# Performance work log

Measured on AMD Instinct MI355X. Metric: run time of the kernel, lower is better.

## Reference

```python
import jax, jax.numpy as jnp
import numpy as np

N, E, F_IN, H, C, G, NC = 10000, 160000, 512, 8, 64, 64, 64


def setup_inputs() -> dict:
    key = jax.random.key(0)
    ks = jax.random.split(key, 16)
    d = {}
    d['x'] = jax.random.normal(ks[0], (N, F_IN), jnp.float32)
    d['edge_index'] = jax.random.randint(ks[1], (2, E), 0, N, dtype=jnp.int32)
    d['batch'] = jnp.sort(jax.random.randint(ks[2], (N,), 0, G, dtype=jnp.int32))
    s = 0.05
    d['enc_W'] = jax.random.normal(ks[3], (F_IN, H * C), jnp.float32) * s
    d['enc_b'] = jnp.zeros((H * C,), jnp.float32)
    d['W1'] = jax.random.normal(ks[4], (H * C, H * C), jnp.float32) * s
    d['as1'] = jax.random.normal(ks[5], (H, C), jnp.float32) * s
    d['ad1'] = jax.random.normal(ks[6], (H, C), jnp.float32) * s
    d['b1'] = jnp.zeros((H * C,), jnp.float32)
    d['g1'] = jnp.ones((H * C,), jnp.float32)
    d['be1'] = jnp.zeros((H * C,), jnp.float32)
    d['W2'] = jax.random.normal(ks[7], (H * C, H * C), jnp.float32) * s
    d['as2'] = jax.random.normal(ks[8], (H, C), jnp.float32) * s
    d['ad2'] = jax.random.normal(ks[9], (H, C), jnp.float32) * s
    d['b2'] = jnp.zeros((H * C,), jnp.float32)
    d['g2'] = jnp.ones((H * C,), jnp.float32)
    d['be2'] = jnp.zeros((H * C,), jnp.float32)
    d['W3'] = jax.random.normal(ks[10], (H * C, C), jnp.float32) * s
    d['as3'] = jax.random.normal(ks[11], (1, C), jnp.float32) * s
    d['ad3'] = jax.random.normal(ks[12], (1, C), jnp.float32) * s
    d['b3'] = jnp.zeros((C,), jnp.float32)
    d['g3'] = jnp.ones((C,), jnp.float32)
    d['be3'] = jnp.zeros((C,), jnp.float32)
    d['lin_W'] = jax.random.normal(ks[13], (C, NC), jnp.float32) * s
    d['lin_b'] = jnp.zeros((NC,), jnp.float32)
    return d


def _gat_conv(x, src, dst, W, a_s, a_d, bias, concat):
    # PyG GATConv (eval mode, self-loops already appended to src/dst)
    n = x.shape[0]
    heads, c = a_s.shape
    h = (x @ W).reshape(n, heads, c)                      # [N,H,C]
    logits = (h * a_s).sum(-1)[src] + (h * a_d).sum(-1)[dst]  # [E',H]
    logits = jax.nn.leaky_relu(logits, 0.2)
    m = jax.ops.segment_max(logits, dst, num_segments=n)  # segment softmax over dst
    e = jnp.exp(logits - m[dst])
    s = jax.ops.segment_sum(e, dst, num_segments=n)
    alpha = e / (s[dst] + 1e-16)                          # [E',H]
    out = jax.ops.segment_sum(alpha[:, :, None] * h[src], dst, num_segments=n)
    out = out.reshape(n, heads * c) if concat else out.mean(axis=1)
    return out + bias


def _bn(x, g, b):
    # BatchNorm1d, training-mode statistics (biased var), eps=1e-5
    mu = x.mean(axis=0)
    var = ((x - mu) ** 2).mean(axis=0)
    return g * (x - mu) / jnp.sqrt(var + 1e-5) + b


def reference(x, edge_index, batch, enc_W, enc_b,
              W1, as1, ad1, b1, g1, be1,
              W2, as2, ad2, b2, g2, be2,
              W3, as3, ad3, b3, g3, be3,
              lin_W, lin_b):
    n = x.shape[0]
    loops = jnp.arange(n, dtype=edge_index.dtype)
    src = jnp.concatenate([edge_index[0], loops])
    dst = jnp.concatenate([edge_index[1], loops])
    x = x @ enc_W + enc_b
    # layer 1 (concat heads) + bn + elu + residual
    h = x
    x = _gat_conv(x, src, dst, W1, as1, ad1, b1, True)
    x = jax.nn.elu(_bn(x, g1, be1))
    x = h + x
    # layer 2
    h = x
    x = _gat_conv(x, src, dst, W2, as2, ad2, b2, True)
    x = jax.nn.elu(_bn(x, g2, be2))
    x = h + x
    # layer 3 (heads=1, mean/no-concat), bn, no elu, no residual (shape mismatch)
    x = _gat_conv(x, src, dst, W3, as3, ad3, b3, False)
    x = _bn(x, g3, be3)
    # global mean pool over graphs
    sums = jax.ops.segment_sum(x, batch, num_segments=G)
    cnt = jax.ops.segment_sum(jnp.ones((n,), x.dtype), batch, num_segments=G)
    xg = sums / jnp.clip(cnt, 1.0)[:, None]
    return xg @ lin_W + lin_b
```

## Files before the change

kernel.cpp:

```cpp
#include <hip/hip_runtime.h>
#include <hip/hip_bf16.h>
#include <math.h>

#define NNODES 10000
#define RPAD   10240
#define MPAD   10112
#define EDGES  160000
#define EPLUS  170000
#define FIN    512
#define HEADS8 8
#define CH     64
#define HC     512
#define NG     64
#define NCLS   64
#define NSTAT  256
#define NSTAT3 64

typedef _Float16 f16x8 __attribute__((ext_vector_type(8)));
typedef _Float16 f16x4 __attribute__((ext_vector_type(4)));
typedef _Float16 f16x2 __attribute__((ext_vector_type(2)));
typedef float    f32x4 __attribute__((ext_vector_type(4)));

#define GLD_LDS16(g, l)                                                        \
    __builtin_amdgcn_global_load_lds(                                          \
        (const __attribute__((address_space(1))) void*)(g),                    \
        (__attribute__((address_space(3))) void*)(l), 16, 0, 0)

#define PREP_CNT  665
#define PREP_CONV 5000
__global__ void prep_all(const int* __restrict__ ei, int* __restrict__ deg,
                         const int* __restrict__ batch, int* __restrict__ goff,
                         const float* __restrict__ x_in, _Float16* __restrict__ x16,
                         const float* __restrict__ Wa, const float* __restrict__ Wb,
                         const float* __restrict__ Wc, const float* __restrict__ Wd,
                         _Float16* __restrict__ Ta, _Float16* __restrict__ Tb,
                         _Float16* __restrict__ Tc, _Float16* __restrict__ Td,
                         _Float16* __restrict__ g16pad, float* __restrict__ g3opad)
{
    const int b   = blockIdx.x;
    const int tid = threadIdx.x;
    if (b < PREP_CNT) {
        const float4 z4 = make_float4(0.f, 0.f, 0.f, 0.f);
        if (b < 60)
            ((float4*)g16pad)[b * 256 + tid] = z4;
        else if (b < 75)
            ((float4*)g3opad)[(b - 60) * 256 + tid] = z4;
        int e = b * 256 + tid;
        if (e < NNODES) {
            int bb = batch[e];
            int bprev = (e == 0) ? -1 : batch[e - 1];
            for (int g = bprev + 1; g <= bb; ++g) goff[g] = e;
            if (e == NNODES - 1)
                for (int g = bb + 1; g <= NG; ++g) goff[g] = NNODES;
        }
        if (e >= EPLUS) return;
        int dst = (e < EDGES) ? ei[EDGES + e] : (e - EDGES);
        atomicAdd(&deg[dst], 1);
    } else if (b < PREP_CNT + PREP_CONV) {
        int i = (b - PREP_CNT) * 256 + tid;
        float4 v = ((const float4*)x_in)[i];
        f16x4 o;
        o[0] = (_Float16)v.x; o[1] = (_Float16)v.y;
        o[2] = (_Float16)v.z; o[3] = (_Float16)v.w;
        ((f16x4*)x16)[i] = o;
    } else {
        int tb = b - (PREP_CNT + PREP_CONV);
        int z  = tb >> 8;
        int rem = tb & 255;
        int bxi = rem & 15, byi = rem >> 4;
        if (z == 3 && bxi >= 2) return;
        const float* W = (z == 0) ? Wa : (z == 1) ? Wb : (z == 2) ? Wc : Wd;
        _Float16*    T = (z == 0) ? Ta : (z == 1) ? Tb : (z == 2) ? Tc : Td;
        const int ldW = (z == 3) ? 64 : 512;
        __shared__ float t[32][33];
        int bx = bxi * 32, by = byi * 32;
        int tx = tid & 31, ty = tid >> 5;
        #pragma unroll
        for (int i = 0; i < 32; i += 8)
            t[ty + i][tx] = W[(size_t)(by + ty + i) * ldW + bx + tx];
        __syncthreads();
        #pragma unroll
        for (int i = 0; i < 32; i += 8)
            T[(size_t)(bx + ty + i) * 512 + by + tx] = (_Float16)t[tx][ty + i];
    }
}

__device__ void exscan_dev(const int* __restrict__ deg, int* __restrict__ off,
                           int* __restrict__ cursor, int* partial )
{
    const int tid = threadIdx.x;
    const int chunk = (NNODES + 255) / 256;
    int begin = tid * chunk;
    int end   = begin + chunk; if (end > NNODES) end = NNODES;
    if (begin > NNODES) begin = NNODES;
    int s = 0;
    for (int i = begin; i < end; ++i) s += deg[i];
    partial[tid] = s;
    __syncthreads();
    for (int o = 1; o < 256; o <<= 1) {
        int v = (tid >= o) ? partial[tid - o] : 0;
        __syncthreads();
        partial[tid] += v;
        __syncthreads();
    }
    int run = (tid > 0) ? partial[tid - 1] : 0;
    for (int i = begin; i < end; ++i) {
        off[i] = run; cursor[i] = run; run += deg[i];
    }
    if (tid == 255) off[NNODES] = run;
}

__global__ __launch_bounds__(256) void gemm_f16_mfma(
    const _Float16* __restrict__ A16, const _Float16* __restrict__ Bt16,
    const float* __restrict__ bias, _Float16* __restrict__ C16,
    float* __restrict__ ssrc, float* __restrict__ sdst,
    const float* __restrict__ a_s, const float* __restrict__ a_d,
    int Mt, int Nn, int K,
    int tail, const int* __restrict__ tp0, int* __restrict__ tp1,
    int* __restrict__ tp2)
{
    __shared__ _Float16 As[128 * 32] __attribute__((aligned(16)));
    __shared__ _Float16 Bs[64 * 32]  __attribute__((aligned(16)));
    __shared__ float sS[2][128];
    __shared__ float sD[2][128];
    const int tid  = threadIdx.x;
    const int ncols = Nn >> 6;
    const int nb    = ncols * (Mt >> 7);
    const int bid   = blockIdx.x;

    if (bid >= nb) {
        if (tail == 1) {
            exscan_dev(tp0, tp1, tp2, (int*)As);
        } else if (tail == 2) {
            int e = (bid - nb) * 256 + tid;
            if (e < EPLUS) {
                int srcN, dstN;
                if (e < EDGES) { srcN = tp0[e]; dstN = tp0[EDGES + e]; }
                else           { srcN = dstN = e - EDGES; }
                int pos = atomicAdd(&tp1[dstN], 1);
                tp2[pos] = srcN;
            }
        }
        return;
    }

    const int bt   = bid % ncols;
    const int row0 = (bid / ncols) * 128;
    const int col0 = bt * 64;
    const int wave = tid >> 6;
    const int lane = tid & 63;
    const int wy = wave >> 1, wx = wave & 1;

    const int lrow = lane >> 2;
    const int lk   = (lane & 3) * 8;

    f32x4 acc[4][2] = {};

    for (int k0 = 0; k0 < K; k0 += 32) {
        if (k0) __syncthreads();
        #pragma unroll
        for (int r = 0; r < 2; ++r) {
            const int chunk = r * 4 + wave;
            const int trow  = chunk * 16 + lrow;
            GLD_LDS16(A16 + (size_t)(row0 + trow) * K + k0 + lk,
                      &As[chunk * 512]);
        }
        {
            const int trow = wave * 16 + lrow;
            GLD_LDS16(Bt16 + (size_t)(col0 + trow) * K + k0 + lk,
                      &Bs[wave * 512]);
        }
        __syncthreads();

        const int quad = lane >> 4;
        const int l16  = lane & 15;
        f16x8 af[4], bf[2];
        #pragma unroll
        for (int m = 0; m < 4; ++m)
            af[m] = *(const f16x8*)&As[(wy * 64 + m * 16 + l16) * 32 + quad * 8];
        #pragma unroll
        for (int n = 0; n < 2; ++n)
            bf[n] = *(const f16x8*)&Bs[(wx * 32 + n * 16 + l16) * 32 + quad * 8];
        #pragma unroll
        for (int m = 0; m < 4; ++m)
            #pragma unroll
            for (int n = 0; n < 2; ++n)
                acc[m][n] = __builtin_amdgcn_mfma_f32_16x16x32_f16(
                    af[m], bf[n], acc[m][n], 0, 0, 0);
    }

    const int quad = lane >> 4;
    const int l16  = lane & 15;
    #pragma unroll
    for (int m = 0; m < 4; ++m) {
        #pragma unroll
        for (int n = 0; n < 2; ++n) {
            const int col = col0 + wx * 32 + n * 16 + l16;
            const float bv = bias ? bias[col] : 0.0f;
            #pragma unroll
            for (int r = 0; r < 4; ++r) {
                const int row = row0 + wy * 64 + m * 16 + quad * 4 + r;
                C16[(size_t)row * Nn + col] = (_Float16)(acc[m][n][r] + bv);
            }
        }
    }

    if (ssrc) {
        float a_sv[2], a_dv[2];
        #pragma unroll
        for (int n = 0; n < 2; ++n) {
            const int col = col0 + wx * 32 + n * 16 + l16;
            a_sv[n] = a_s[col & 511];
            a_dv[n] = a_d[col & 511];
        }
        #pragma unroll
        for (int m = 0; m < 4; ++m) {
            #pragma unroll
            for (int r = 0; r < 4; ++r) {
                float vs = acc[m][0][r] * a_sv[0] + acc[m][1][r] * a_sv[1];
                float vd = acc[m][0][r] * a_dv[0] + acc[m][1][r] * a_dv[1];
                vs += __shfl_xor(vs, 1); vs += __shfl_xor(vs, 2);
                vs += __shfl_xor(vs, 4); vs += __shfl_xor(vs, 8);
                vd += __shfl_xor(vd, 1); vd += __shfl_xor(vd, 2);
                vd += __shfl_xor(vd, 4); vd += __shfl_xor(vd, 8);
                if (l16 == 0) {
                    const int lr = wy * 64 + m * 16 + quad * 4 + r;
                    sS[wx][lr] = vs;
                    sD[wx][lr] = vd;
                }
            }
        }
        __syncthreads();
        if (wx == 0 && l16 == 0) {
            const int head = bt;
            #pragma unroll
            for (int m = 0; m < 4; ++m)
                #pragma unroll
                for (int r = 0; r < 4; ++r) {
                    const int lr = wy * 64 + m * 16 + quad * 4 + r;
                    const int row = row0 + lr;
                    ssrc[(size_t)row * HEADS8 + head] = sS[0][lr] + sS[1][lr];
                    sdst[(size_t)row * HEADS8 + head] = sD[0][lr] + sD[1][lr];
                }
        }
    }
}

__global__ __launch_bounds__(256) void gemm_f16_mfma_n64(
    const _Float16* __restrict__ A16, const _Float16* __restrict__ Bt16,
    _Float16* __restrict__ C16,
    float* __restrict__ ssrc, float* __restrict__ sdst,
    const float* __restrict__ a_s, const float* __restrict__ a_d)
{
    __shared__ _Float16 As[64 * 32] __attribute__((aligned(16)));
    __shared__ _Float16 Bs[64 * 32] __attribute__((aligned(16)));
    __shared__ float sS[2][64];
    __shared__ float sD[2][64];
    const int tid  = threadIdx.x;
    const int wave = tid >> 6;
    const int lane = tid & 63;
    const int row0 = blockIdx.x * 64;
    const int wy = wave >> 1, wx = wave & 1;

    const int lrow = lane >> 2;
    const int lk   = (lane & 3) * 8;

    f32x4 acc[2][2] = {};

    for (int k0 = 0; k0 < 512; k0 += 32) {
        if (k0) __syncthreads();
        {
            const int trow = wave * 16 + lrow;
            GLD_LDS16(A16 + (size_t)(row0 + trow) * 512 + k0 + lk, &As[wave * 512]);
            GLD_LDS16(Bt16 + (size_t)trow * 512 + k0 + lk, &Bs[wave * 512]);
        }
        __syncthreads();

        const int quad = lane >> 4;
        const int l16  = lane & 15;
        f16x8 af[2], bf[2];
        #pragma unroll
        for (int m = 0; m < 2; ++m)
            af[m] = *(const f16x8*)&As[(wy * 32 + m * 16 + l16) * 32 + quad * 8];
        #pragma unroll
        for (int n = 0; n < 2; ++n)
            bf[n] = *(const f16x8*)&Bs[(wx * 32 + n * 16 + l16) * 32 + quad * 8];
        #pragma unroll
        for (int m = 0; m < 2; ++m)
            #pragma unroll
            for (int n = 0; n < 2; ++n)
                acc[m][n] = __builtin_amdgcn_mfma_f32_16x16x32_f16(
                    af[m], bf[n], acc[m][n], 0, 0, 0);
    }

    const int quad = lane >> 4;
    const int l16  = lane & 15;
    #pragma unroll
    for (int m = 0; m < 2; ++m)
        #pragma unroll
        for (int n = 0; n < 2; ++n) {
            const int col = wx * 32 + n * 16 + l16;
            #pragma unroll
            for (int r = 0; r < 4; ++r) {
                const int row = row0 + wy * 32 + m * 16 + quad * 4 + r;
                C16[(size_t)row * 64 + col] = (_Float16)acc[m][n][r];
            }
        }

    {
        float a_sv[2], a_dv[2];
        #pragma unroll
        for (int n = 0; n < 2; ++n) {
            const int col = wx * 32 + n * 16 + l16;
            a_sv[n] = a_s[col];
            a_dv[n] = a_d[col];
        }
        #pragma unroll
        for (int m = 0; m < 2; ++m)
            #pragma unroll
            for (int r = 0; r < 4; ++r) {
                float vs = acc[m][0][r] * a_sv[0] + acc[m][1][r] * a_sv[1];
                float vd = acc[m][0][r] * a_dv[0] + acc[m][1][r] * a_dv[1];
                vs += __shfl_xor(vs, 1); vs += __shfl_xor(vs, 2);
                vs += __shfl_xor(vs, 4); vs += __shfl_xor(vs, 8);
                vd += __shfl_xor(vd, 1); vd += __shfl_xor(vd, 2);
                vd += __shfl_xor(vd, 4); vd += __shfl_xor(vd, 8);
                if (l16 == 0) {
                    const int lr = wy * 32 + m * 16 + quad * 4 + r;
                    sS[wx][lr] = vs;
                    sD[wx][lr] = vd;
                }
            }
        __syncthreads();
        if (wx == 0 && l16 == 0) {
            #pragma unroll
            for (int m = 0; m < 2; ++m)
                #pragma unroll
                for (int r = 0; r < 4; ++r) {
                    const int lr = wy * 32 + m * 16 + quad * 4 + r;
                    const int row = row0 + lr;
                    ssrc[row] = sS[0][lr] + sS[1][lr];
                    sdst[row] = sD[0][lr] + sD[1][lr];
                }
        }
    }
}

__global__ __launch_bounds__(64) void gat_aggregate8(
    const _Float16* __restrict__ Hf, const float* __restrict__ ssrc,
    const float* __restrict__ sdst, const int* __restrict__ off,
    const int* __restrict__ csr, const float* __restrict__ bias,
    _Float16* __restrict__ out)
{
    const int n    = blockIdx.x;
    const int lane = threadIdx.x;
    const int head = lane >> 3;
    const int e0 = off[n], e1 = off[n + 1];

    float4 sd0 = ((const float4*)(sdst + n * 8))[0];
    float4 sd1 = ((const float4*)(sdst + n * 8))[1];
    float sd[8] = {sd0.x, sd0.y, sd0.z, sd0.w, sd1.x, sd1.y, sd1.z, sd1.w};

    __shared__ float exL[64 * 8];
    __shared__ int   srcL[64];
    float acc[8]  = {};
    float ssum[8] = {};
    for (int base = e0; base < e1; base += 64) {
        int cnt = e1 - base; if (cnt > 64) cnt = 64;
        if (lane < cnt) {
            int s = csr[base + lane];
            srcL[lane] = s;
            float4 s0 = ((const float4*)(ssrc + s * 8))[0];
            float4 s1 = ((const float4*)(ssrc + s * 8))[1];
            float lv[8] = {s0.x, s0.y, s0.z, s0.w, s1.x, s1.y, s1.z, s1.w};
            #pragma unroll
            for (int h = 0; h < 8; ++h) {
                float l = lv[h] + sd[h];
                l = (l > 0.f) ? l : 0.2f * l;
                float ex = __expf(l);
                exL[lane * 8 + h] = ex;
                ssum[h] += ex;
            }
        }
        __syncthreads();
        int j = 0;
        for (; j + 4 <= cnt; j += 4) {
            const int s0 = srcL[j],     s1 = srcL[j + 1];
            const int s2 = srcL[j + 2], s3 = srcL[j + 3];
            f16x8 h0 = *(const f16x8*)(Hf + (size_t)s0 * HC + lane * 8);
            f16x8 h1 = *(const f16x8*)(Hf + (size_t)s1 * HC + lane * 8);
            f16x8 h2 = *(const f16x8*)(Hf + (size_t)s2 * HC + lane * 8);
            f16x8 h3 = *(const f16x8*)(Hf + (size_t)s3 * HC + lane * 8);
            const float a0 = exL[(j)     * 8 + head];
            const float a1 = exL[(j + 1) * 8 + head];
            const float a2 = exL[(j + 2) * 8 + head];
            const float a3 = exL[(j + 3) * 8 + head];
            #pragma unroll
            for (int c = 0; c < 8; ++c) {
                acc[c] = fmaf(a0, (float)h0[c], acc[c]);
                acc[c] = fmaf(a1, (float)h1[c], acc[c]);
                acc[c] = fmaf(a2, (float)h2[c], acc[c]);
                acc[c] = fmaf(a3, (float)h3[c], acc[c]);
            }
        }
        for (; j < cnt; ++j) {
            const int s = srcL[j];
            f16x8 hv = *(const f16x8*)(Hf + (size_t)s * HC + lane * 8);
            const float al = exL[j * 8 + head];
            #pragma unroll
            for (int c = 0; c < 8; ++c)
                acc[c] = fmaf(al, (float)hv[c], acc[c]);
        }
        __syncthreads();
    }
    #pragma unroll
    for (int h = 0; h < 8; ++h)
        #pragma unroll
        for (int o = 1; o < 64; o <<= 1)
            ssum[h] += __shfl_xor(ssum[h], o);

    const float inv = 1.0f / (ssum[head] + 1e-16f);
    const float* bp = bias + lane * 8;
    f16x8 ov;
    #pragma unroll
    for (int c = 0; c < 8; ++c)
        ov[c] = (_Float16)(acc[c] * inv + bp[c]);
    *(f16x8*)(out + (size_t)n * HC + lane * 8) = ov;
}

__global__ __launch_bounds__(64) void gat_aggregate1(
    const _Float16* __restrict__ Hf, const float* __restrict__ ssrc,
    const float* __restrict__ sdst, const int* __restrict__ off,
    const int* __restrict__ csr, const float* __restrict__ bias,
    float* __restrict__ out)
{
    const int n    = blockIdx.x;
    const int lane = threadIdx.x;
    const int e0 = off[n], e1 = off[n + 1];
    const float sd = sdst[n];

    __shared__ float exL[64];
    __shared__ int   srcL[64];
    float acc = 0.f, ssum = 0.f;
    for (int base = e0; base < e1; base += 64) {
        int cnt = e1 - base; if (cnt > 64) cnt = 64;
        if (lane < cnt) {
            int s = csr[base + lane];
            srcL[lane] = s;
            float l = ssrc[s] + sd;
            l = (l > 0.f) ? l : 0.2f * l;
            float ex = __expf(l);
            exL[lane] = ex;
            ssum += ex;
        }
        __syncthreads();
        int j = 0;
        for (; j + 4 <= cnt; j += 4) {
            const int s0 = srcL[j],     s1 = srcL[j + 1];
            const int s2 = srcL[j + 2], s3 = srcL[j + 3];
            float h0 = (float)Hf[(size_t)s0 * 64 + lane];
            float h1 = (float)Hf[(size_t)s1 * 64 + lane];
            float h2 = (float)Hf[(size_t)s2 * 64 + lane];
            float h3 = (float)Hf[(size_t)s3 * 64 + lane];
            acc = fmaf(exL[j],     h0, acc);
            acc = fmaf(exL[j + 1], h1, acc);
            acc = fmaf(exL[j + 2], h2, acc);
            acc = fmaf(exL[j + 3], h3, acc);
        }
        for (; j < cnt; ++j)
            acc = fmaf(exL[j], (float)Hf[(size_t)srcL[j] * 64 + lane], acc);
        __syncthreads();
    }
    #pragma unroll
    for (int o = 1; o < 64; o <<= 1)
        ssum += __shfl_xor(ssum, o);

    out[(size_t)n * 64 + lane] = acc / (ssum + 1e-16f) + bias[lane];
}

__global__ __launch_bounds__(256) void bn_stats_f16(
    const _Float16* __restrict__ x,
    float* __restrict__ psum, float* __restrict__ psq)
{
    const int t    = threadIdx.x;
    const int lane = t & 63;
    const int wv   = t >> 6;
    const int w    = blockIdx.x * 4 + wv;
    float s[8] = {}, q[8] = {};
    #pragma unroll
    for (int k = 0; k < RPAD / 2048; ++k) {
        const int r0 = w + k * 2048;
        f16x8 v0 = *(const f16x8*)(x + (size_t)r0 * HC + lane * 8);
        f16x8 v1 = *(const f16x8*)(x + (size_t)(r0 + 1024) * HC + lane * 8);
        #pragma unroll
        for (int j = 0; j < 8; ++j) {
            float f0 = (float)v0[j], f1 = (float)v1[j];
            s[j] += f0 + f1;
            q[j] += f0 * f0 + f1 * f1;
        }
    }
    __shared__ float ls[4][HC];
    __shared__ float lq[4][HC];
    #pragma unroll
    for (int j = 0; j < 8; ++j) {
        ls[wv][lane * 8 + j] = s[j];
        lq[wv][lane * 8 + j] = q[j];
    }
    __syncthreads();
    const size_t bo = (size_t)blockIdx.x * HC;
    #pragma unroll
    for (int k = 0; k < 2; ++k) {
        const int ch = t + k * 256;
        psum[bo + ch] = ls[0][ch] + ls[1][ch] + ls[2][ch] + ls[3][ch];
        psq [bo + ch] = lq[0][ch] + lq[1][ch] + lq[2][ch] + lq[3][ch];
    }
}

__global__ __launch_bounds__(256) void bn_stats3(
    const float* __restrict__ x,
    float* __restrict__ psum, float* __restrict__ psq)
{
    const int t    = threadIdx.x;
    const int c4   = (t & 15) * 4;
    const int rsub = t >> 4;
    float s[4] = {}, q[4] = {};
    #pragma unroll
    for (int k = 0; k < RPAD / 1024; ++k) {
        const int r = blockIdx.x * 16 + rsub + k * 1024;
        float4 v = *(const float4*)(x + (size_t)r * CH + c4);
        s[0] += v.x; q[0] += v.x * v.x;
        s[1] += v.y; q[1] += v.y * v.y;
        s[2] += v.z; q[2] += v.z * v.z;
        s[3] += v.w; q[3] += v.w * v.w;
    }
    __shared__ float ls[16][CH];
    __shared__ float lq[16][CH];
    #pragma unroll
    for (int j = 0; j < 4; ++j) {
        ls[rsub][c4 + j] = s[j];
        lq[rsub][c4 + j] = q[j];
    }
    __syncthreads();
    if (t < CH) {
        float tot = 0.f;
        #pragma unroll
        for (int p = 0; p < 16; ++p) tot += ls[p][t];
        psum[(size_t)blockIdx.x * CH + t] = tot;
    } else if (t < 2 * CH) {
        const int ch = t - CH;
        float tot = 0.f;
        #pragma unroll
        for (int p = 0; p < 16; ++p) tot += lq[p][ch];
        psq[(size_t)blockIdx.x * CH + ch] = tot;
    }
}

__global__ __launch_bounds__(256) void bn_finalize(
    const float* __restrict__ psum, const float* __restrict__ psq,
    const float* __restrict__ g, const float* __restrict__ be,
    float* __restrict__ scale, float* __restrict__ shift,
    float invN, int cols, int np)
{
    const int t  = threadIdx.x;
    const int pg = t >> 4;
    const int cl = t & 15;
    const int ch = blockIdx.x * 16 + cl;
    float S = 0.f, Q = 0.f;
    for (int p = pg; p < np; p += 16) {
        S += psum[(size_t)p * cols + ch];
        Q += psq [(size_t)p * cols + ch];
    }
    __shared__ float lsS[16][16];
    __shared__ float lsQ[16][16];
    lsS[pg][cl] = S;
    lsQ[pg][cl] = Q;
    __syncthreads();
    if (t < 16) {
        float S2 = 0.f, Q2 = 0.f;
        #pragma unroll
        for (int p = 0; p < 16; ++p) { S2 += lsS[p][t]; Q2 += lsQ[p][t]; }
        const int c = blockIdx.x * 16 + t;
        float mu  = S2 * invN;
        float var = Q2 * invN - mu * mu;
        float sc  = g[c] / sqrtf(var + 1e-5f);
        scale[c] = sc;
        shift[c] = be[c] - mu * sc;
    }
}

__global__ void bn_apply16(const _Float16* __restrict__ xin,
                           const _Float16* __restrict__ res,
                           const float* __restrict__ scale,
                           const float* __restrict__ shift,
                           _Float16* __restrict__ out, size_t total8)
{
    size_t i = (size_t)blockIdx.x * blockDim.x + threadIdx.x;
    if (i >= total8) return;
    int c = (int)((i * 8) & (size_t)(HC - 1));
    f16x8 xv = ((const f16x8*)xin)[i];
    f16x8 rv = ((const f16x8*)res)[i];
    float4 sa = *(const float4*)(scale + c);
    float4 sb = *(const float4*)(scale + c + 4);
    float4 ha = *(const float4*)(shift + c);
    float4 hb = *(const float4*)(shift + c + 4);
    float sc[8] = {sa.x, sa.y, sa.z, sa.w, sb.x, sb.y, sb.z, sb.w};
    float sh[8] = {ha.x, ha.y, ha.z, ha.w, hb.x, hb.y, hb.z, hb.w};
    f16x8 o;
    #pragma unroll
    for (int j = 0; j < 8; ++j) {
        float v = (float)xv[j] * sc[j] + sh[j];
        v = (v > 0.f) ? v : expm1f(v);
        o[j] = (_Float16)(v + (float)rv[j]);
    }
    ((f16x8*)out)[i] = o;
}

__global__ __launch_bounds__(256) void pool_linear(
    const float* __restrict__ x, const int* __restrict__ goff,
    const float* __restrict__ W, const float* __restrict__ b,
    const float* __restrict__ scale, const float* __restrict__ shift,
    float* __restrict__ out)
{
    const int g    = blockIdx.x;
    const int lane = threadIdx.x & 63;
    const int wave = threadIdx.x >> 6;
    const int r0 = goff[g], r1 = goff[g + 1];
    float s = 0.f;
    for (int r = r0 + wave; r < r1; r += 4)
        s += x[(size_t)r * CH + lane];
    __shared__ float red[4][CH];
    __shared__ float mean_l[CH];
    red[wave][lane] = s;
    __syncthreads();
    if (wave == 0) {
        float tot = red[0][lane] + red[1][lane] + red[2][lane] + red[3][lane];
        float cnt = (float)(r1 - r0);
        float m = tot / fmaxf(cnt, 1.0f);
        mean_l[lane] = m * scale[lane] + shift[lane];
    }
    __syncthreads();
    if (threadIdx.x < NCLS) {
        const int j = threadIdx.x;
        float acc = b[j];
        for (int c = 0; c < CH; ++c)
            acc = fmaf(mean_l[c], W[c * NCLS + j], acc);
        out[g * NCLS + j] = acc;
    }
}

extern "C" void kernel_launch(void* const* d_in, const int* in_sizes, int n_in,
                              void* d_out, int out_size, void* d_ws, size_t ws_size,
                              hipStream_t stream)
{
    const float* x_in  = (const float*)d_in[0];
    const int*   ei    = (const int*)  d_in[1];
    const int*   batch = (const int*)  d_in[2];
    const float* enc_W = (const float*)d_in[3];
    const float* enc_b = (const float*)d_in[4];
    const float* W1  = (const float*)d_in[5];
    const float* as1 = (const float*)d_in[6];
    const float* ad1 = (const float*)d_in[7];
    const float* b1  = (const float*)d_in[8];
    const float* g1  = (const float*)d_in[9];
    const float* be1 = (const float*)d_in[10];
    const float* W2  = (const float*)d_in[11];
    const float* as2 = (const float*)d_in[12];
    const float* ad2 = (const float*)d_in[13];
    const float* b2  = (const float*)d_in[14];
    const float* g2  = (const float*)d_in[15];
    const float* be2 = (const float*)d_in[16];
    const float* W3  = (const float*)d_in[17];
    const float* as3 = (const float*)d_in[18];
    const float* ad3 = (const float*)d_in[19];
    const float* b3  = (const float*)d_in[20];
    const float* g3  = (const float*)d_in[21];
    const float* be3 = (const float*)d_in[22];
    const float* linW = (const float*)d_in[23];
    const float* linb = (const float*)d_in[24];
    float* out = (float*)d_out;

    char* ws = (char*)d_ws;
    size_t off_b = 0;
    auto alloc = [&](size_t bytes) -> void* {
        void* p = ws + off_b;
        off_b = (off_b + bytes + 255) & ~(size_t)255;
        return p;
    };
    _Float16* f16A   = (_Float16*)alloc((size_t)MPAD * HC * 2);
    _Float16* f16B   = (_Float16*)alloc((size_t)MPAD * HC * 2);
    _Float16* H16    = (_Float16*)alloc((size_t)MPAD * HC * 2);
    _Float16* g16    = (_Float16*)alloc((size_t)RPAD * HC * 2);
    _Float16* h3_16  = (_Float16*)alloc((size_t)MPAD * CH * 2);
    float*    g3o    = (float*)alloc((size_t)RPAD * CH * 4);
    _Float16* encWt  = (_Float16*)alloc((size_t)HC * FIN * 2);
    _Float16* W1t    = (_Float16*)alloc((size_t)HC * HC * 2);
    _Float16* W2t    = (_Float16*)alloc((size_t)HC * HC * 2);
    _Float16* W3t    = (_Float16*)alloc((size_t)CH * HC * 2);
    float* ssrc   = (float*)alloc((size_t)MPAD * HEADS8 * 4);
    float* sdst   = (float*)alloc((size_t)MPAD * HEADS8 * 4);
    int*   deg    = (int*)  alloc((size_t)NNODES * 4);
    int*   offp   = (int*)  alloc((size_t)(NNODES + 1) * 4);
    int*   cursor = (int*)  alloc((size_t)NNODES * 4);
    int*   csr    = (int*)  alloc((size_t)EPLUS * 4);
    int*   goff   = (int*)  alloc((size_t)(NG + 1) * 4);
    float* psum   = (float*)alloc((size_t)NSTAT * HC * 4);
    float* psq    = (float*)alloc((size_t)NSTAT * HC * 4);
    float* psum3  = (float*)alloc((size_t)NSTAT3 * CH * 4);
    float* psq3   = (float*)alloc((size_t)NSTAT3 * CH * 4);
    float* bnsc   = (float*)alloc(HC * 4);
    float* bnsh   = (float*)alloc(HC * 4);

    hipMemsetAsync(deg, 0, (size_t)NNODES * 4, stream);
    prep_all<<<PREP_CNT + PREP_CONV + 1024, 256, 0, stream>>>(
        ei, deg, batch, goff, x_in, f16A, enc_W, W1, W2, W3,
        encWt, W1t, W2t, W3t,
        g16 + (size_t)NNODES * HC, g3o + (size_t)NNODES * CH);

    const int NB = (HC / 64) * (MPAD / 128);
    const int SCAT = (EPLUS + 255) / 256;

    gemm_f16_mfma<<<NB + 1, 256, 0, stream>>>(
        f16A, encWt, enc_b, f16B, nullptr, nullptr, nullptr, nullptr,
        MPAD, HC, FIN, 1, deg, offp, cursor);

    const size_t total8 = (size_t)NNODES * HC / 8;
    const int apply_blocks = (int)((total8 + 255) / 256);
    const float invN = 1.0f / NNODES;

    gemm_f16_mfma<<<NB + SCAT, 256, 0, stream>>>(
        f16B, W1t, nullptr, H16, ssrc, sdst, as1, ad1,
        MPAD, HC, HC, 2, ei, cursor, csr);
    gat_aggregate8<<<NNODES, 64, 0, stream>>>(H16, ssrc, sdst, offp, csr,
                                              b1, g16);
    bn_stats_f16<<<NSTAT, 256, 0, stream>>>(g16, psum, psq);
    bn_finalize<<<HC / 16, 256, 0, stream>>>(psum, psq, g1, be1, bnsc, bnsh,
                                             invN, HC, NSTAT);
    bn_apply16<<<apply_blocks, 256, 0, stream>>>(g16, f16B, bnsc, bnsh,
                                                 f16A, total8);

    gemm_f16_mfma<<<NB, 256, 0, stream>>>(
        f16A, W2t, nullptr, H16, ssrc, sdst, as2, ad2,
        MPAD, HC, HC, 0, nullptr, nullptr, nullptr);
    gat_aggregate8<<<NNODES, 64, 0, stream>>>(H16, ssrc, sdst, offp, csr,
                                              b2, g16);
    bn_stats_f16<<<NSTAT, 256, 0, stream>>>(g16, psum, psq);
    bn_finalize<<<HC / 16, 256, 0, stream>>>(psum, psq, g2, be2, bnsc, bnsh,
                                             invN, HC, NSTAT);
    bn_apply16<<<apply_blocks, 256, 0, stream>>>(g16, f16A, bnsc, bnsh,
                                                 f16B, total8);

    gemm_f16_mfma_n64<<<MPAD / 64, 256, 0, stream>>>(f16B, W3t, h3_16,
                                                     ssrc, sdst, as3, ad3);
    gat_aggregate1<<<NNODES, 64, 0, stream>>>(h3_16, ssrc, sdst, offp, csr,
                                              b3, g3o);
    bn_stats3<<<NSTAT3, 256, 0, stream>>>(g3o, psum3, psq3);
    bn_finalize<<<CH / 16, 256, 0, stream>>>(psum3, psq3, g3, be3, bnsc, bnsh,
                                             invN, CH, NSTAT3);

    pool_linear<<<NG, 256, 0, stream>>>(g3o, goff, linW, linb, bnsc, bnsh,
                                        out);
}
```

Before: 323.8 us.

## Widen GEMM tile to 128 columns and unroll aggregation gather by eight

The MFMA GEMM tile grows from 128x64 to 128x128 so each wave computes a full 64-column head. Per-head attention scores can then be reduced within a wave and written directly, which drops the shared-memory staging and the extra barrier. The aggregation kernel gains an 8-way unrolled gather loop so more neighbour feature loads are in flight at once. The trade-off is half as many GEMM blocks (fewer waves to fill the GPU) and higher register pressure from the 4x4 accumulators and the 8 loaded vectors.

```diff
diff --git a/kernel.cpp b/kernel.cpp
--- a/kernel.cpp
+++ b/kernel.cpp
@@ -120,11 +120,9 @@
     int* __restrict__ tp2)
 {
     __shared__ _Float16 As[128 * 32] __attribute__((aligned(16)));
-    __shared__ _Float16 Bs[64 * 32]  __attribute__((aligned(16)));
-    __shared__ float sS[2][128];
-    __shared__ float sD[2][128];
+    __shared__ _Float16 Bs[128 * 32] __attribute__((aligned(16)));
     const int tid  = threadIdx.x;
-    const int ncols = Nn >> 6;
+    const int ncols = Nn >> 7;
     const int nb    = ncols * (Mt >> 7);
     const int bid   = blockIdx.x;
 
@@ -146,7 +144,7 @@
 
     const int bt   = bid % ncols;
     const int row0 = (bid / ncols) * 128;
-    const int col0 = bt * 64;
+    const int col0 = bt * 128;
     const int wave = tid >> 6;
     const int lane = tid & 63;
     const int wy = wave >> 1, wx = wave & 1;
@@ -154,7 +152,7 @@
     const int lrow = lane >> 2;
     const int lk   = (lane & 3) * 8;
 
-    f32x4 acc[4][2] = {};
+    f32x4 acc[4][4] = {};
 
     for (int k0 = 0; k0 < K; k0 += 32) {
         if (k0) __syncthreads();
@@ -164,27 +162,24 @@
             const int trow  = chunk * 16 + lrow;
             GLD_LDS16(A16 + (size_t)(row0 + trow) * K + k0 + lk,
                       &As[chunk * 512]);
-        }
-        {
-            const int trow = wave * 16 + lrow;
             GLD_LDS16(Bt16 + (size_t)(col0 + trow) * K + k0 + lk,
-                      &Bs[wave * 512]);
+                      &Bs[chunk * 512]);
         }
         __syncthreads();
 
         const int quad = lane >> 4;
         const int l16  = lane & 15;
-        f16x8 af[4], bf[2];
+        f16x8 af[4], bf[4];
         #pragma unroll
         for (int m = 0; m < 4; ++m)
             af[m] = *(const f16x8*)&As[(wy * 64 + m * 16 + l16) * 32 + quad * 8];
         #pragma unroll
-        for (int n = 0; n < 2; ++n)
-            bf[n] = *(const f16x8*)&Bs[(wx * 32 + n * 16 + l16) * 32 + quad * 8];
+        for (int n = 0; n < 4; ++n)
+            bf[n] = *(const f16x8*)&Bs[(wx * 64 + n * 16 + l16) * 32 + quad * 8];
         #pragma unroll
         for (int m = 0; m < 4; ++m)
             #pragma unroll
-            for (int n = 0; n < 2; ++n)
+            for (int n = 0; n < 4; ++n)
                 acc[m][n] = __builtin_amdgcn_mfma_f32_16x16x32_f16(
                     af[m], bf[n], acc[m][n], 0, 0, 0);
     }
@@ -194,8 +189,8 @@
     #pragma unroll
     for (int m = 0; m < 4; ++m) {
         #pragma unroll
-        for (int n = 0; n < 2; ++n) {
-            const int col = col0 + wx * 32 + n * 16 + l16;
+        for (int n = 0; n < 4; ++n) {
+            const int col = col0 + wx * 64 + n * 16 + l16;
             const float bv = bias ? bias[col] : 0.0f;
             #pragma unroll
             for (int r = 0; r < 4; ++r) {
@@ -206,10 +201,11 @@
     }
 
     if (ssrc) {
-        float a_sv[2], a_dv[2];
-        #pragma unroll
-        for (int n = 0; n < 2; ++n) {
-            const int col = col0 + wx * 32 + n * 16 + l16;
+        const int head = bt * 2 + wx;
+        float a_sv[4], a_dv[4];
+        #pragma unroll
+        for (int n = 0; n < 4; ++n) {
+            const int col = col0 + wx * 64 + n * 16 + l16;
             a_sv[n] = a_s[col & 511];
             a_dv[n] = a_d[col & 511];
         }
@@ -217,31 +213,20 @@
         for (int m = 0; m < 4; ++m) {
             #pragma unroll
             for (int r = 0; r < 4; ++r) {
-                float vs = acc[m][0][r] * a_sv[0] + acc[m][1][r] * a_sv[1];
-                float vd = acc[m][0][r] * a_dv[0] + acc[m][1][r] * a_dv[1];
+                float vs = acc[m][0][r] * a_sv[0] + acc[m][1][r] * a_sv[1]
+                         + acc[m][2][r] * a_sv[2] + acc[m][3][r] * a_sv[3];
+                float vd = acc[m][0][r] * a_dv[0] + acc[m][1][r] * a_dv[1]
+                         + acc[m][2][r] * a_dv[2] + acc[m][3][r] * a_dv[3];
                 vs += __shfl_xor(vs, 1); vs += __shfl_xor(vs, 2);
                 vs += __shfl_xor(vs, 4); vs += __shfl_xor(vs, 8);
                 vd += __shfl_xor(vd, 1); vd += __shfl_xor(vd, 2);
                 vd += __shfl_xor(vd, 4); vd += __shfl_xor(vd, 8);
                 if (l16 == 0) {
-                    const int lr = wy * 64 + m * 16 + quad * 4 + r;
-                    sS[wx][lr] = vs;
-                    sD[wx][lr] = vd;
+                    const int row = row0 + wy * 64 + m * 16 + quad * 4 + r;
+                    ssrc[(size_t)row * HEADS8 + head] = vs;
+                    sdst[(size_t)row * HEADS8 + head] = vd;
                 }
             }
-        }
-        __syncthreads();
-        if (wx == 0 && l16 == 0) {
-            const int head = bt;
-            #pragma unroll
-            for (int m = 0; m < 4; ++m)
-                #pragma unroll
-                for (int r = 0; r < 4; ++r) {
-                    const int lr = wy * 64 + m * 16 + quad * 4 + r;
-                    const int row = row0 + lr;
-                    ssrc[(size_t)row * HEADS8 + head] = sS[0][lr] + sS[1][lr];
-                    sdst[(size_t)row * HEADS8 + head] = sD[0][lr] + sD[1][lr];
-                }
         }
     }
 }
@@ -384,6 +369,19 @@
         }
         __syncthreads();
         int j = 0;
+        for (; j + 8 <= cnt; j += 8) {
+            f16x8 hv[8];
+            #pragma unroll
+            for (int u = 0; u < 8; ++u)
+                hv[u] = *(const f16x8*)(Hf + (size_t)srcL[j + u] * HC + lane * 8);
+            #pragma unroll
+            for (int u = 0; u < 8; ++u) {
+                const float a = exL[(j + u) * 8 + head];
+                #pragma unroll
+                for (int c = 0; c < 8; ++c)
+                    acc[c] = fmaf(a, (float)hv[u][c], acc[c]);
+            }
+        }
         for (; j + 4 <= cnt; j += 4) {
             const int s0 = srcL[j],     s1 = srcL[j + 1];
             const int s2 = srcL[j + 2], s3 = srcL[j + 3];
@@ -716,7 +714,7 @@
         encWt, W1t, W2t, W3t,
         g16 + (size_t)NNODES * HC, g3o + (size_t)NNODES * CH);
 
-    const int NB = (HC / 64) * (MPAD / 128);
+    const int NB = (HC / 128) * (MPAD / 128);
     const int SCAT = (EPLUS + 255) / 256;
 
     gemm_f16_mfma<<<NB + 1, 256, 0, stream>>>(
```

Result: faster. 313.5 us (-3.2%).
